# Kernel optimization log

Hardware: AMD Instinct MI355X
Metric: run time of the kernel (lower is better)

The kernel has to match this reference:

```python
import jax, jax.numpy as jnp
import numpy as np

B, S, D, H = 4, 2048, 1024, 16
HD = D // H  # head dim = 64


def setup_inputs() -> dict:
    key = jax.random.key(0)
    k1, k2, k3 = jax.random.split(key, 3)
    scale = 1.0 / np.sqrt(D).astype(np.float32)
    x = jax.random.normal(k1, (B, S, D), dtype=jnp.float32)
    # q/k slices of nn.MultiheadAttention's in_proj (v and out_proj never
    # influence the returned values since x_t is discarded by forward)
    wq = jax.random.normal(k2, (D, D), dtype=jnp.float32) * scale
    wk = jax.random.normal(k3, (D, D), dtype=jnp.float32) * scale
    bq = jnp.zeros((D,), dtype=jnp.float32)
    bk = jnp.zeros((D,), dtype=jnp.float32)
    # 8 contiguous scale blocks of 256 tokens; last boundary == S
    scales_idx = (jnp.arange(1, 9, dtype=jnp.int64) * (S // 8))
    return {"x": x, "wq": wq, "wk": wk, "bq": bq, "bk": bk,
            "scales_idx": scales_idx}


def reference(x, wq, wk, bq, bk, scales_idx):
    b, s, d = x.shape
    # project q, k and split heads: [B, H, S, HD]
    q = (x @ wq.T + bq).reshape(b, s, H, HD).transpose(0, 2, 1, 3)
    k = (x @ wk.T + bk).reshape(b, s, H, HD).transpose(0, 2, 1, 3)
    inv_sqrt_hd = jnp.asarray(1.0 / np.sqrt(HD), dtype=x.dtype)
    scores = jnp.einsum('bhqd,bhkd->bhqk', q, k) * inv_sqrt_hd  # [B,H,S,S]
    # block-diagonal mask: token i belongs to the block whose right boundary
    # is the first scales_idx entry strictly greater than i
    pos = jnp.arange(s)
    seg = jnp.searchsorted(scales_idx, pos, side='right')  # [S]
    allowed = seg[:, None] == seg[None, :]                  # [S,S] bool
    scores = jnp.where(allowed[None, None], scores, -jnp.inf)
    w = jax.nn.softmax(scores, axis=-1)  # every row has >=1 allowed entry
    weights_attn = jnp.mean(w, axis=1)   # average over heads -> [B,S,S]
    return (x, weights_attn)
```

## Files before the change

### kernel.cpp

```cpp
#include <hip/hip_runtime.h>
#include <hip/hip_bf16.h>
#include <math.h>

#define BB 4
#define SS 2048
#define DD 1024
#define HH 16
#define HD 64
#define MM (BB*SS)
#define NN (2*DD)

typedef __attribute__((ext_vector_type(8))) short short8;
typedef __attribute__((ext_vector_type(4))) float f32x4;
typedef unsigned short ushort_t;

__device__ __forceinline__ void gload16(const void* g, void* l) {
    __builtin_amdgcn_global_load_lds((const __attribute__((address_space(1))) unsigned int*)g,
                                     (__attribute__((address_space(3))) unsigned int*)l,
                                     16, 0, 0);
}

__global__ __launch_bounds__(256)
void copy_cast(const float* __restrict__ x, float* __restrict__ out_x,
               __hip_bfloat16* __restrict__ xb, int n8)
{
    int i = blockIdx.x * 256 + threadIdx.x;
    if (i >= n8) return;
    const float4* s = (const float4*)x + (size_t)i * 2;
    float4 a = s[0], b = s[1];
    float4* o = (float4*)out_x + (size_t)i * 2;
    o[0] = a; o[1] = b;
    __hip_bfloat16 tmp[8];
    tmp[0] = __float2bfloat16(a.x); tmp[1] = __float2bfloat16(a.y);
    tmp[2] = __float2bfloat16(a.z); tmp[3] = __float2bfloat16(a.w);
    tmp[4] = __float2bfloat16(b.x); tmp[5] = __float2bfloat16(b.y);
    tmp[6] = __float2bfloat16(b.z); tmp[7] = __float2bfloat16(b.w);
    *(float4*)&xb[(size_t)i * 8] = *(float4*)tmp;
}

__global__ __launch_bounds__(256)
void cast_w(const float* __restrict__ wq, const float* __restrict__ wk,
            __hip_bfloat16* __restrict__ wb)
{
    const int half = (DD * DD) / 8;
    int i = blockIdx.x * 256 + threadIdx.x;
    if (i >= 2 * half) return;
    const float* src = (i < half) ? wq : wk;
    int j = (i < half) ? i : i - half;
    const float4* s = (const float4*)src + (size_t)j * 2;
    float4 a = s[0], b = s[1];
    __hip_bfloat16 tmp[8];
    tmp[0] = __float2bfloat16(a.x); tmp[1] = __float2bfloat16(a.y);
    tmp[2] = __float2bfloat16(a.z); tmp[3] = __float2bfloat16(a.w);
    tmp[4] = __float2bfloat16(b.x); tmp[5] = __float2bfloat16(b.y);
    tmp[6] = __float2bfloat16(b.z); tmp[7] = __float2bfloat16(b.w);
    *(float4*)&wb[(size_t)i * 8] = *(float4*)tmp;
}

__global__ __launch_bounds__(256, 2)
void proj_mfma(const ushort_t* __restrict__ xb, const ushort_t* __restrict__ wb,
               const float* __restrict__ bq, const float* __restrict__ bk,
               __hip_bfloat16* __restrict__ Qb, __hip_bfloat16* __restrict__ Kb)
{
    __shared__ __align__(16) ushort_t As[128 * 64];
    __shared__ __align__(16) ushort_t Bs[128 * 64];

    const int t = threadIdx.x;
    const int wv = t >> 6, lane = t & 63, quad = lane >> 4, l15 = lane & 15;
    const int m0 = blockIdx.x * 128, n0 = blockIdx.y * 128;
    const int wm = (wv & 1) * 64, wn = (wv >> 1) * 64;

    f32x4 acc[4][4];
    #pragma unroll
    for (int mt = 0; mt < 4; ++mt)
        #pragma unroll
        for (int nt = 0; nt < 4; ++nt) acc[mt][nt] = (f32x4){0.f, 0.f, 0.f, 0.f};

    for (int kt = 0; kt < DD; kt += 64) {
        __syncthreads();
        #pragma unroll
        for (int call = 0; call < 4; ++call) {
            int c = call * 256 + t;
            int row = c >> 3, ch = c & 7;
            int gch = ch ^ (row & 7);
            gload16(xb + (size_t)(m0 + row) * DD + kt + gch * 8,
                    As + ((size_t)call * 256 + wv * 64) * 8);
            gload16(wb + (size_t)(n0 + row) * DD + kt + gch * 8,
                    Bs + ((size_t)call * 256 + wv * 64) * 8);
        }
        __syncthreads();
        #pragma unroll
        for (int ks = 0; ks < 2; ++ks) {
            short8 a[4], bb_[4];
            #pragma unroll
            for (int mt = 0; mt < 4; ++mt) {
                int r = wm + mt * 16 + l15;
                int sl = r * 8 + ((ks * 4 + quad) ^ (r & 7));
                a[mt] = *(const short8*)&As[sl * 8];
            }
            #pragma unroll
            for (int nt = 0; nt < 4; ++nt) {
                int r = wn + nt * 16 + l15;
                int sl = r * 8 + ((ks * 4 + quad) ^ (r & 7));
                bb_[nt] = *(const short8*)&Bs[sl * 8];
            }
            #pragma unroll
            for (int mt = 0; mt < 4; ++mt)
                #pragma unroll
                for (int nt = 0; nt < 4; ++nt)
                    acc[mt][nt] = __builtin_amdgcn_mfma_f32_16x16x32_bf16(
                        a[mt], bb_[nt], acc[mt][nt], 0, 0, 0);
        }
    }

    const bool isQ = (n0 < DD);
    const float* bias = isQ ? bq : bk;
    __hip_bfloat16* outp = isQ ? Qb : Kb;
    const int nc0 = isQ ? n0 : (n0 - DD);
    #pragma unroll
    for (int nt = 0; nt < 4; ++nt) {
        const int nc = nc0 + wn + nt * 16 + l15;
        const float bv = bias[nc];
        #pragma unroll
        for (int mt = 0; mt < 4; ++mt)
            #pragma unroll
            for (int reg = 0; reg < 4; ++reg) {
                int m = m0 + wm + mt * 16 + quad * 4 + reg;
                outp[(size_t)m * DD + nc] = __float2bfloat16(acc[mt][nt][reg] + bv);
            }
    }
}

__global__ __launch_bounds__(256, 1)
void attn_block(const ushort_t* __restrict__ Qb, const ushort_t* __restrict__ Kb,
                const int* __restrict__ scales, float* __restrict__ outw)
{
    __shared__ __align__(16) char smem[73728];
    ushort_t* KsB = (ushort_t*)smem;
    ushort_t* QsB = (ushort_t*)(smem + 65536);
    float (*comb)[256] = (float(*)[256])smem;

    const int bid = blockIdx.x;
    const int rt = bid & 7, blk = (bid >> 3) & 7, bb = bid >> 6;
    const int start = blk ? scales[blk - 1] : 0;

    const int t = threadIdx.x;
    const int wv = t >> 6, lane = t & 63, quad = lane >> 4, l15 = lane & 15;
    const int rg = wv & 1, hg = wv >> 1;

    f32x4 accm[16];
    #pragma unroll
    for (int nt = 0; nt < 16; ++nt) accm[nt] = (f32x4){0.f, 0.f, 0.f, 0.f};

    const int qrow0 = start + rt * 32;

    for (int i = 0; i < 8; ++i) {
        __syncthreads();
        #pragma unroll
        for (int half = 0; half < 2; ++half) {
            const int h = half * 8 + i;
            ushort_t* Kl = KsB + half * (256 * 64);
            ushort_t* Ql = QsB + half * (32 * 64);
            #pragma unroll
            for (int round = 0; round < 8; ++round) {
                int c = round * 256 + t;
                int row = c >> 3, ch = c & 7;
                int gch = ch ^ (row & 7);
                gload16(Kb + (size_t)(bb * SS + start + row) * DD + h * HD + gch * 8,
                        Kl + ((size_t)round * 256 + wv * 64) * 8);
            }
            {
                int row = t >> 3, ch = t & 7;
                int gch = ch ^ (row & 7);
                gload16(Qb + (size_t)(bb * SS + qrow0 + row) * DD + h * HD + gch * 8,
                        Ql + ((size_t)wv * 64) * 8);
            }
        }
        __syncthreads();

        const ushort_t* Ks = KsB + hg * (256 * 64);
        const ushort_t* Qs = QsB + hg * (32 * 64);

        short8 af[2];
        #pragma unroll
        for (int ks = 0; ks < 2; ++ks) {
            int qr = rg * 16 + l15;
            int sl = qr * 8 + ((ks * 4 + quad) ^ (qr & 7));
            af[ks] = *(const short8*)&Qs[sl * 8];
        }
        f32x4 sc[16];
        #pragma unroll
        for (int nt = 0; nt < 16; ++nt) {
            sc[nt] = (f32x4){0.f, 0.f, 0.f, 0.f};
            #pragma unroll
            for (int ks = 0; ks < 2; ++ks) {
                int kr = nt * 16 + l15;
                int sl = kr * 8 + ((ks * 4 + quad) ^ (kr & 7));
                short8 bf = *(const short8*)&Ks[sl * 8];
                sc[nt] = __builtin_amdgcn_mfma_f32_16x16x32_bf16(af[ks], bf, sc[nt], 0, 0, 0);
            }
        }
        float rs[4] = {0.f, 0.f, 0.f, 0.f};
        #pragma unroll
        for (int nt = 0; nt < 16; ++nt) {
            #pragma unroll
            for (int r = 0; r < 4; ++r) {
                float p = __expf(sc[nt][r] * 0.125f);
                sc[nt][r] = p;
                rs[r] += p;
            }
        }
        #pragma unroll
        for (int r = 0; r < 4; ++r) {
            #pragma unroll
            for (int off = 1; off < 16; off <<= 1) rs[r] += __shfl_xor(rs[r], off, 64);
            rs[r] = 1.0f / rs[r];
        }
        #pragma unroll
        for (int nt = 0; nt < 16; ++nt)
            #pragma unroll
            for (int r = 0; r < 4; ++r) accm[nt][r] += sc[nt][r] * rs[r];
    }

    __syncthreads();
    if (hg == 0) {
        #pragma unroll
        for (int nt = 0; nt < 16; ++nt)
            #pragma unroll
            for (int r = 0; r < 4; ++r)
                comb[rg * 16 + quad * 4 + r][nt * 16 + l15] = accm[nt][r];
    }
    __syncthreads();
    if (hg == 1) {
        #pragma unroll
        for (int nt = 0; nt < 16; ++nt)
            #pragma unroll
            for (int r = 0; r < 4; ++r)
                comb[rg * 16 + quad * 4 + r][nt * 16 + l15] += accm[nt][r];
    }
    __syncthreads();

    const float s16 = 1.0f / (float)HH;
    const size_t orow0 = (size_t)bb * SS + qrow0;
    #pragma unroll
    for (int it = 0; it < 64; ++it) {
        int flat = it * 256 + t;
        int row = flat >> 9;
        int col = (flat & 511) * 4;
        float4 v = make_float4(0.f, 0.f, 0.f, 0.f);
        unsigned lc = (unsigned)(col - start);
        if (lc < 256u) {
            const float* c = &comb[row][lc];
            v = make_float4(c[0] * s16, c[1] * s16, c[2] * s16, c[3] * s16);
        }
        *(float4*)&outw[(orow0 + row) * SS + col] = v;
    }
}

extern "C" void kernel_launch(void* const* d_in, const int* in_sizes, int n_in,
                              void* d_out, int out_size, void* d_ws, size_t ws_size,
                              hipStream_t stream)
{
    const float* x  = (const float*)d_in[0];
    const float* wq = (const float*)d_in[1];
    const float* wk = (const float*)d_in[2];
    const float* bq = (const float*)d_in[3];
    const float* bk = (const float*)d_in[4];
    const int* scales = (const int*)d_in[5];

    float* out_x = (float*)d_out;
    float* out_w = out_x + (size_t)BB * SS * DD;

    char* w = (char*)d_ws;
    __hip_bfloat16* xb = (__hip_bfloat16*)(w);
    __hip_bfloat16* wb = (__hip_bfloat16*)(w + 16777216);
    __hip_bfloat16* Qb = (__hip_bfloat16*)(w + 20971520);
    __hip_bfloat16* Kb = (__hip_bfloat16*)(w + 37748736);

    copy_cast<<<4096, 256, 0, stream>>>(x, out_x, xb, (MM * DD) / 8);
    cast_w<<<1024, 256, 0, stream>>>(wq, wk, wb);

    dim3 pgrid(MM / 128, NN / 128);
    proj_mfma<<<pgrid, 256, 0, stream>>>((const ushort_t*)xb, (const ushort_t*)wb,
                                         bq, bk, Qb, Kb);

    attn_block<<<256, 256, 0, stream>>>((const ushort_t*)Qb, (const ushort_t*)Kb,
                                        scales, out_w);
}
```

Measured before the change: 212.4 us.

## Rewrite projection GEMM as 256x256 double-buffered 8-wave pipelined MFMA kernel

The projection GEMM moves from 128x128 tiles with 4 waves and a single LDS buffer to 256x256 tiles with 8 waves and double-buffered LDS. Each k-step is split into four quarter phases, and each phase interleaves an async global-to-LDS stage of the next tile with MFMA work, using s_setprio and explicit waitcnt barriers. The aim is to hide load latency and raise arithmetic intensity. The attention kernel's block index mapping is also reordered so consecutive blocks cover different batch/scale blocks. The cost is heavier LDS use (128KB) and fragile hand-written wait counts.

```diff
diff --git a/kernel.cpp b/kernel.cpp
--- a/kernel.cpp
+++ b/kernel.cpp
@@ -9,6 +9,8 @@
 #define HD 64
 #define MM (BB*SS)
 #define NN (2*DD)
+#define BK 64
+#define NKT 16
 
 typedef __attribute__((ext_vector_type(8))) short short8;
 typedef __attribute__((ext_vector_type(4))) float f32x4;
@@ -57,75 +59,184 @@
     *(float4*)&wb[(size_t)i * 8] = *(float4*)tmp;
 }
 
-__global__ __launch_bounds__(256, 2)
+__device__ __forceinline__ void stage_A(const ushort_t* __restrict__ xb, ushort_t* Ab,
+                                        int m0, int kt, int mh, int wv, int lane)
+{
+    #pragma unroll
+    for (int it = 0; it < 2; ++it) {
+        int rl0 = it * 64 + wv * 8;
+        int r0 = (rl0 & 63) + ((rl0 >> 6) << 7) + mh * 64;
+        int r  = r0 + (lane >> 3);
+        int gch = (lane & 7) ^ (r & 7);
+        gload16(xb + (size_t)(m0 + r) * DD + kt + gch * 8, Ab + r0 * 64);
+    }
+}
+
+__device__ __forceinline__ void stage_Bt(const ushort_t* __restrict__ wb, ushort_t* Bb,
+                                         int n0, int kt, int nh, int wv, int lane)
+{
+    #pragma unroll
+    for (int it = 0; it < 2; ++it) {
+        int rl0 = it * 64 + wv * 8;
+        int r0 = (rl0 & 31) + ((rl0 >> 5) << 6) + nh * 32;
+        int r  = r0 + (lane >> 3);
+        int gch = (lane & 7) ^ (r & 7);
+        gload16(wb + (size_t)(n0 + r) * DD + kt + gch * 8, Bb + r0 * 64);
+    }
+}
+
+__global__ __launch_bounds__(512, 2)
 void proj_mfma(const ushort_t* __restrict__ xb, const ushort_t* __restrict__ wb,
                const float* __restrict__ bq, const float* __restrict__ bk,
                __hip_bfloat16* __restrict__ Qb, __hip_bfloat16* __restrict__ Kb)
 {
-    __shared__ __align__(16) ushort_t As[128 * 64];
-    __shared__ __align__(16) ushort_t Bs[128 * 64];
+    __shared__ __align__(16) ushort_t As[2][256 * BK];
+    __shared__ __align__(16) ushort_t Bs[2][256 * BK];
 
     const int t = threadIdx.x;
     const int wv = t >> 6, lane = t & 63, quad = lane >> 4, l15 = lane & 15;
-    const int m0 = blockIdx.x * 128, n0 = blockIdx.y * 128;
-    const int wm = (wv & 1) * 64, wn = (wv >> 1) * 64;
-
-    f32x4 acc[4][4];
-    #pragma unroll
-    for (int mt = 0; mt < 4; ++mt)
+    const int wr = wv >> 2, wc = wv & 3;
+    const int m0 = blockIdx.x * 256, n0 = blockIdx.y * 256;
+
+    f32x4 acc[8][4];
+    #pragma unroll
+    for (int mt = 0; mt < 8; ++mt)
         #pragma unroll
         for (int nt = 0; nt < 4; ++nt) acc[mt][nt] = (f32x4){0.f, 0.f, 0.f, 0.f};
 
-    for (int kt = 0; kt < DD; kt += 64) {
-        __syncthreads();
-        #pragma unroll
-        for (int call = 0; call < 4; ++call) {
-            int c = call * 256 + t;
-            int row = c >> 3, ch = c & 7;
-            int gch = ch ^ (row & 7);
-            gload16(xb + (size_t)(m0 + row) * DD + kt + gch * 8,
-                    As + ((size_t)call * 256 + wv * 64) * 8);
-            gload16(wb + (size_t)(n0 + row) * DD + kt + gch * 8,
-                    Bs + ((size_t)call * 256 + wv * 64) * 8);
-        }
-        __syncthreads();
-        #pragma unroll
-        for (int ks = 0; ks < 2; ++ks) {
-            short8 a[4], bb_[4];
-            #pragma unroll
-            for (int mt = 0; mt < 4; ++mt) {
-                int r = wm + mt * 16 + l15;
+    stage_Bt(wb, Bs[0], n0, 0, 0, wv, lane);
+    stage_A (xb, As[0], m0, 0, 0, wv, lane);
+    stage_A (xb, As[0], m0, 0, 1, wv, lane);
+    stage_Bt(wb, Bs[0], n0, 0, 1, wv, lane);
+    stage_Bt(wb, Bs[1], n0, BK, 0, wv, lane);
+    stage_A (xb, As[1], m0, BK, 0, wv, lane);
+    asm volatile("s_waitcnt vmcnt(4)" ::: "memory");
+    __builtin_amdgcn_s_barrier();
+
+    #pragma unroll 1
+    for (int tt = 0; tt < NKT; ++tt) {
+        ushort_t* Ac = As[tt & 1];
+        ushort_t* Bc = Bs[tt & 1];
+        ushort_t* An = As[(tt & 1) ^ 1];
+        ushort_t* Bn = Bs[(tt & 1) ^ 1];
+        short8 a[8][2], b[2][2];
+
+        #pragma unroll
+        for (int mt = 0; mt < 4; ++mt)
+            #pragma unroll
+            for (int ks = 0; ks < 2; ++ks) {
+                int r = wr * 128 + mt * 16 + l15;
                 int sl = r * 8 + ((ks * 4 + quad) ^ (r & 7));
-                a[mt] = *(const short8*)&As[sl * 8];
-            }
-            #pragma unroll
-            for (int nt = 0; nt < 4; ++nt) {
-                int r = wn + nt * 16 + l15;
+                a[mt][ks] = *(const short8*)&Ac[sl * 8];
+            }
+        #pragma unroll
+        for (int nt = 0; nt < 2; ++nt)
+            #pragma unroll
+            for (int ks = 0; ks < 2; ++ks) {
+                int r = wc * 64 + nt * 16 + l15;
                 int sl = r * 8 + ((ks * 4 + quad) ^ (r & 7));
-                bb_[nt] = *(const short8*)&Bs[sl * 8];
-            }
-            #pragma unroll
-            for (int mt = 0; mt < 4; ++mt)
+                b[nt][ks] = *(const short8*)&Bc[sl * 8];
+            }
+        if (tt + 1 < NKT) stage_A(xb, An, m0, (tt + 1) * BK, 1, wv, lane);
+        __builtin_amdgcn_s_barrier();
+        asm volatile("s_waitcnt lgkmcnt(0)" ::: "memory");
+        __builtin_amdgcn_sched_barrier(0);
+        __builtin_amdgcn_s_setprio(1);
+        #pragma unroll
+        for (int mt = 0; mt < 4; ++mt)
+            #pragma unroll
+            for (int nt = 0; nt < 2; ++nt)
                 #pragma unroll
-                for (int nt = 0; nt < 4; ++nt)
+                for (int ks = 0; ks < 2; ++ks)
                     acc[mt][nt] = __builtin_amdgcn_mfma_f32_16x16x32_bf16(
-                        a[mt], bb_[nt], acc[mt][nt], 0, 0, 0);
-        }
+                        a[mt][ks], b[nt][ks], acc[mt][nt], 0, 0, 0);
+        __builtin_amdgcn_s_setprio(0);
+        __builtin_amdgcn_sched_barrier(0);
+        __builtin_amdgcn_s_barrier();
+
+        #pragma unroll
+        for (int mt = 0; mt < 4; ++mt)
+            #pragma unroll
+            for (int ks = 0; ks < 2; ++ks) {
+                int r = wr * 128 + 64 + mt * 16 + l15;
+                int sl = r * 8 + ((ks * 4 + quad) ^ (r & 7));
+                a[4 + mt][ks] = *(const short8*)&Ac[sl * 8];
+            }
+        if (tt + 1 < NKT) stage_Bt(wb, Bn, n0, (tt + 1) * BK, 1, wv, lane);
+        __builtin_amdgcn_s_barrier();
+        asm volatile("s_waitcnt lgkmcnt(0)" ::: "memory");
+        __builtin_amdgcn_sched_barrier(0);
+        __builtin_amdgcn_s_setprio(1);
+        #pragma unroll
+        for (int mt = 0; mt < 4; ++mt)
+            #pragma unroll
+            for (int nt = 0; nt < 2; ++nt)
+                #pragma unroll
+                for (int ks = 0; ks < 2; ++ks)
+                    acc[4 + mt][nt] = __builtin_amdgcn_mfma_f32_16x16x32_bf16(
+                        a[4 + mt][ks], b[nt][ks], acc[4 + mt][nt], 0, 0, 0);
+        __builtin_amdgcn_s_setprio(0);
+        __builtin_amdgcn_sched_barrier(0);
+        __builtin_amdgcn_s_barrier();
+
+        #pragma unroll
+        for (int nt = 0; nt < 2; ++nt)
+            #pragma unroll
+            for (int ks = 0; ks < 2; ++ks) {
+                int r = wc * 64 + 32 + nt * 16 + l15;
+                int sl = r * 8 + ((ks * 4 + quad) ^ (r & 7));
+                b[nt][ks] = *(const short8*)&Bc[sl * 8];
+            }
+        if (tt + 2 < NKT) stage_Bt(wb, Bc, n0, (tt + 2) * BK, 0, wv, lane);
+        __builtin_amdgcn_s_barrier();
+        asm volatile("s_waitcnt lgkmcnt(0)" ::: "memory");
+        __builtin_amdgcn_sched_barrier(0);
+        __builtin_amdgcn_s_setprio(1);
+        #pragma unroll
+        for (int mt = 0; mt < 4; ++mt)
+            #pragma unroll
+            for (int nt = 0; nt < 2; ++nt)
+                #pragma unroll
+                for (int ks = 0; ks < 2; ++ks)
+                    acc[mt][2 + nt] = __builtin_amdgcn_mfma_f32_16x16x32_bf16(
+                        a[mt][ks], b[nt][ks], acc[mt][2 + nt], 0, 0, 0);
+        __builtin_amdgcn_s_setprio(0);
+        __builtin_amdgcn_sched_barrier(0);
+        __builtin_amdgcn_s_barrier();
+
+        if (tt + 2 < NKT) stage_A(xb, Ac, m0, (tt + 2) * BK, 0, wv, lane);
+        __builtin_amdgcn_s_barrier();
+        asm volatile("s_waitcnt lgkmcnt(0)" ::: "memory");
+        __builtin_amdgcn_sched_barrier(0);
+        __builtin_amdgcn_s_setprio(1);
+        #pragma unroll
+        for (int mt = 0; mt < 4; ++mt)
+            #pragma unroll
+            for (int nt = 0; nt < 2; ++nt)
+                #pragma unroll
+                for (int ks = 0; ks < 2; ++ks)
+                    acc[4 + mt][2 + nt] = __builtin_amdgcn_mfma_f32_16x16x32_bf16(
+                        a[4 + mt][ks], b[nt][ks], acc[4 + mt][2 + nt], 0, 0, 0);
+        __builtin_amdgcn_s_setprio(0);
+        __builtin_amdgcn_sched_barrier(0);
+        if (tt < NKT - 2)       asm volatile("s_waitcnt vmcnt(4)" ::: "memory");
+        else if (tt == NKT - 2) asm volatile("s_waitcnt vmcnt(0)" ::: "memory");
+        __builtin_amdgcn_s_barrier();
     }
 
     const bool isQ = (n0 < DD);
     const float* bias = isQ ? bq : bk;
     __hip_bfloat16* outp = isQ ? Qb : Kb;
-    const int nc0 = isQ ? n0 : (n0 - DD);
+    const int nc0 = (isQ ? n0 : n0 - DD) + wc * 64;
     #pragma unroll
     for (int nt = 0; nt < 4; ++nt) {
-        const int nc = nc0 + wn + nt * 16 + l15;
+        const int nc = nc0 + nt * 16 + l15;
         const float bv = bias[nc];
         #pragma unroll
-        for (int mt = 0; mt < 4; ++mt)
+        for (int mt = 0; mt < 8; ++mt)
             #pragma unroll
             for (int reg = 0; reg < 4; ++reg) {
-                int m = m0 + wm + mt * 16 + quad * 4 + reg;
+                int m = m0 + wr * 128 + mt * 16 + quad * 4 + reg;
                 outp[(size_t)m * DD + nc] = __float2bfloat16(acc[mt][nt][reg] + bv);
             }
     }
@@ -141,7 +252,8 @@
     float (*comb)[256] = (float(*)[256])smem;
 
     const int bid = blockIdx.x;
-    const int rt = bid & 7, blk = (bid >> 3) & 7, bb = bid >> 6;
+    const int rt  = bid >> 5;
+    const int blk = bid & 7, bb = (bid >> 3) & 3;
     const int start = blk ? scales[blk - 1] : 0;
 
     const int t = threadIdx.x;
@@ -280,8 +392,8 @@
     copy_cast<<<4096, 256, 0, stream>>>(x, out_x, xb, (MM * DD) / 8);
     cast_w<<<1024, 256, 0, stream>>>(wq, wk, wb);
 
-    dim3 pgrid(MM / 128, NN / 128);
-    proj_mfma<<<pgrid, 256, 0, stream>>>((const ushort_t*)xb, (const ushort_t*)wb,
+    dim3 pgrid(MM / 256, NN / 256);
+    proj_mfma<<<pgrid, 512, 0, stream>>>((const ushort_t*)xb, (const ushort_t*)wb,
                                          bq, bk, Qb, Kb);
 
     attn_block<<<256, 256, 0, stream>>>((const ushort_t*)Qb, (const ushort_t*)Kb,
```

After: 208.0 us. -2.0%, faster.
